# Optimization experiments

Hardware: AMD Instinct MI355X
Metric: run time of the kernel (lower is better)

Reference implementation:

```python
import jax, jax.numpy as jnp
import numpy as np

B, T, D, E, K = 4, 1024, 512, 10, 2
H = 4 * D          # expert hidden
CITY, CE = 8, 32   # num cities, city embedding dim
LIN = D + CE + D // 4 + D // 4 + D // 8 + D // 8  # 928 router input dim


def setup_inputs() -> dict:
    key = jax.random.key(0)
    ks = jax.random.split(key, 16)
    s = 0.02  # init scale for weights
    return {
        "x": jax.random.normal(ks[0], (B, T, D), jnp.float32),
        "delta_t": jax.random.normal(ks[1], (B, T, D // 4), jnp.float32),
        "delta_dis": jax.random.normal(ks[2], (B, T, D // 4), jnp.float32),
        "delta_rg": jax.random.normal(ks[3], (B, T, D // 8), jnp.float32),
        "delta_entropy": jax.random.normal(ks[4], (B, T, D // 8), jnp.float32),
        "city_emb": jax.random.normal(ks[5], (CITY, CE), jnp.float32),
        "Wg": jax.random.normal(ks[6], (E, LIN), jnp.float32) * s,
        "bg": jnp.zeros((E,), jnp.float32),
        "Wn": jax.random.normal(ks[7], (E, LIN), jnp.float32) * s,
        "bn": jnp.zeros((E,), jnp.float32),
        "W1": jax.random.normal(ks[8], (E, D, H), jnp.float32) * s,
        "b1": jnp.zeros((E, H), jnp.float32),
        "W2": jax.random.normal(ks[9], (E, H, D), jnp.float32) * s,
        "b2": jnp.zeros((E, D), jnp.float32),
        "noise": jax.random.normal(ks[10], (B, T, E), jnp.float32),
        "city": jax.random.randint(ks[11], (B,), 0, CITY),
    }


def reference(x, delta_t, delta_dis, delta_rg, delta_entropy, city_emb,
              Wg, bg, Wn, bn, W1, b1, W2, b2, noise, city):
    # ---- router: concat features -> noisy top-k gating ----
    ce = city_emb[city]                                   # (B, CE)
    ce = jnp.broadcast_to(ce[:, None, :], (x.shape[0], x.shape[1], ce.shape[-1]))
    h = jnp.concatenate([x, ce, delta_t, delta_dis, delta_rg, delta_entropy], axis=-1)  # (B,T,LIN)
    logits = jnp.einsum('btl,el->bte', h, Wg) + bg        # clean gate logits
    gate1 = jax.nn.softmax(logits, axis=-1)               # dense gate (returned for aux loss)
    noise_logits = jnp.einsum('btl,el->bte', h, Wn) + bn
    noisy = logits + noise * jax.nn.softplus(noise_logits)
    _, idx = jax.lax.top_k(noisy, K)                      # (B,T,K)
    sel = jax.nn.one_hot(idx, E, dtype=noisy.dtype).sum(-2) > 0  # (B,T,E) bool
    gating = jax.nn.softmax(jnp.where(sel, noisy, -jnp.inf), axis=-1)  # zeros off top-k

    # ---- experts: dense compute, combine weighted by sparse gate ----
    flat_x = x.reshape(-1, D)                             # (N, D)
    flat_g = gating.reshape(-1, E)                        # (N, E), zero for non-selected
    hid = jax.nn.gelu(jnp.einsum('nd,edh->neh', flat_x, W1) + b1, approximate=False)
    y = jnp.einsum('neh,ehd->ned', hid, W2) + b2          # (N, E, D)
    out = jnp.einsum('ne,ned->nd', flat_g, y).reshape(x.shape)
    return out, gate1
```

## Files before the change

### kernel.cpp

```cpp
#include <hip/hip_runtime.h>
#include <hip/hip_bf16.h>

#define B_      4
#define T_      1024
#define NTOK    4096
#define D_      512
#define E_      10
#define H_      2048
#define LIN_    928
#define TOPK    2
#define BM      128
#define ROWS_CAP 9472
#define TILES_CAP 74

typedef __bf16 bf16x8 __attribute__((ext_vector_type(8)));
typedef float  f32x4  __attribute__((ext_vector_type(4)));
typedef unsigned short ushort8 __attribute__((ext_vector_type(8)));

#define OFF_W1T   0ull
#define SZ_W1T    (10ull*2048*512*2)
#define OFF_W2T   (OFF_W1T + SZ_W1T)
#define SZ_W2T    SZ_W1T
#define OFF_XG    (OFF_W2T + SZ_W2T)
#define SZ_XG     ((size_t)ROWS_CAP*512*2)
#define OFF_HID   (OFF_XG + SZ_XG)
#define SZ_HID    ((size_t)ROWS_CAP*2048*2)
#define OFF_Y     OFF_W1T
#define OFF_TOKE  (OFF_HID + SZ_HID)
#define OFF_TOKG  (OFF_TOKE + 32768)
#define OFF_TROWS (OFF_TOKG + 32768)
#define OFF_RANK  (OFF_TROWS + 32768)
#define OFF_CNT   (OFF_RANK + 32768)
#define OFF_OFFS  (OFF_CNT + 64)
#define OFF_TE    (OFF_OFFS + 64)
#define OFF_TR    (OFF_TE + 512)

static __device__ __forceinline__ unsigned short f2b(float f) {
  unsigned int u = __float_as_uint(f);
  unsigned int r = (u + 0x7fffu + ((u >> 16) & 1u)) >> 16;
  return (unsigned short)r;
}

static __device__ __forceinline__ float b2f(unsigned short u) {
  return __uint_as_float(((unsigned int)u) << 16);
}

static __device__ __forceinline__ void gld16(const void* g, void* l) {
  __builtin_amdgcn_global_load_lds(
      (const __attribute__((address_space(1))) unsigned int*)g,
      (__attribute__((address_space(3))) unsigned int*)l, 16, 0, 0);
}

struct WconvLds { float t[64][65]; };

static __device__ __forceinline__ void wconv_body(
    const float* __restrict__ src, unsigned short* __restrict__ dst,
    int R, int C, int e, int bx, int by, int tid, WconvLds* W) {
  int c0 = bx << 6, r0 = by << 6;
  int rr = tid >> 4, cc = (tid & 15) << 2;
  const float* s = src + ((size_t)e * R + r0 + rr) * C + c0 + cc;
#pragma unroll
  for (int p = 0; p < 4; p++) {
    float4 v = *(const float4*)(s + (size_t)p * 16 * C);
    W->t[rr + p * 16][cc + 0] = v.x; W->t[rr + p * 16][cc + 1] = v.y;
    W->t[rr + p * 16][cc + 2] = v.z; W->t[rr + p * 16][cc + 3] = v.w;
  }
  __syncthreads();
  int wc2 = tid >> 2;
  unsigned short* d = dst + ((size_t)e * C + c0 + wc2) * R + r0;
#pragma unroll
  for (int p = 0; p < 4; p++) {
    int rb = ((tid & 3) << 2) + (p << 4);
    ushort4 o;
    o.x = f2b(W->t[rb + 0][wc2]); o.y = f2b(W->t[rb + 1][wc2]);
    o.z = f2b(W->t[rb + 2][wc2]); o.w = f2b(W->t[rb + 3][wc2]);
    *(ushort4*)&d[rb] = o;
  }
}

__global__ __launch_bounds__(256) void prep_k(
    const float* __restrict__ x, const float* __restrict__ dt,
    const float* __restrict__ dd, const float* __restrict__ dr,
    const float* __restrict__ de, const float* __restrict__ cemb,
    const int* __restrict__ city,
    const float* __restrict__ Wg, const float* __restrict__ Wn,
    const float* __restrict__ bg, const float* __restrict__ bn,
    const float* __restrict__ noise,
    const float* __restrict__ W1, const float* __restrict__ W2,
    unsigned short* __restrict__ w1T, unsigned short* __restrict__ w2T,
    float* __restrict__ gate1, int* __restrict__ tok_e,
    float* __restrict__ tok_g, int* __restrict__ ranks,
    int* __restrict__ counts) {
  __shared__ WconvLds W;
  __shared__ int lcnt[E_], lbase[E_];
  int bx = blockIdx.x;
  int tid = threadIdx.x;
  if (bx >= 256) {
    int idx = bx - 256;
    if (idx < 2560) wconv_body(W1, w1T, 512, 2048, idx / 256, idx & 31, (idx >> 5) & 7, tid, &W);
    else { idx -= 2560; wconv_body(W2, w2T, 2048, 512, idx / 256, idx & 7, (idx >> 3) & 31, tid, &W); }
    return;
  }
  if (tid < E_) lcnt[tid] = 0;
  __syncthreads();
  int lane = tid & 63;
  int gw = bx * 4 + (tid >> 6);
  int n0 = gw * 4;
  int cb = city[n0 >> 10];

  float acc[4][20];
#pragma unroll
  for (int j = 0; j < 4; j++)
#pragma unroll
    for (int o = 0; o < 20; o++) acc[j][o] = 0.f;

  {
    float hce = (lane < 32) ? cemb[cb * 32 + lane] : 0.f;
    int c = 512 + (lane & 31);
#pragma unroll
    for (int o = 0; o < 10; o++) {
      float wg = Wg[o * LIN_ + c];
      float wn = Wn[o * LIN_ + c];
#pragma unroll
      for (int j = 0; j < 4; j++) {
        acc[j][o]      = fmaf(hce, wg, acc[j][o]);
        acc[j][10 + o] = fmaf(hce, wn, acc[j][10 + o]);
      }
    }
  }
#pragma unroll
  for (int s = 0; s < 5; s++) {
    const float* hp; int Wd, cofs;
    if      (s == 0) { hp = x;  Wd = 512; cofs = 0;   }
    else if (s == 1) { hp = dt; Wd = 128; cofs = 544; }
    else if (s == 2) { hp = dd; Wd = 128; cofs = 672; }
    else if (s == 3) { hp = dr; Wd = 64;  cofs = 800; }
    else             { hp = de; Wd = 64;  cofs = 864; }
    for (int base = 0; base < Wd; base += 64) {
      int c = cofs + base + lane;
      float wv[20];
#pragma unroll
      for (int o = 0; o < 10; o++) {
        wv[o]      = Wg[o * LIN_ + c];
        wv[10 + o] = Wn[o * LIN_ + c];
      }
      float hv[4];
#pragma unroll
      for (int j = 0; j < 4; j++) hv[j] = hp[(size_t)(n0 + j) * Wd + base + lane];
#pragma unroll
      for (int j = 0; j < 4; j++)
#pragma unroll
        for (int o = 0; o < 20; o++) acc[j][o] = fmaf(hv[j], wv[o], acc[j][o]);
    }
  }
#pragma unroll
  for (int off = 1; off < 64; off <<= 1) {
#pragma unroll
    for (int j = 0; j < 4; j++)
#pragma unroll
      for (int o = 0; o < 20; o++) acc[j][o] += __shfl_xor(acc[j][o], off);
  }
  float sv[20];
#pragma unroll
  for (int o = 0; o < 20; o++) {
    float v = acc[0][o];
    v = (lane == 1) ? acc[1][o] : v;
    v = (lane == 2) ? acc[2][o] : v;
    v = (lane == 3) ? acc[3][o] : v;
    sv[o] = v;
  }
  int n = n0 + lane;
  int i0 = 0, i1 = 0, rr0 = 0, rr1 = 0;
  float gg0 = 0.f, gg1 = 0.f, gate[E_];
#pragma unroll
  for (int o = 0; o < E_; o++) gate[o] = 0.f;
  if (lane < 4) {
    float logits[E_], noisy[E_];
    float mx = -3.4e38f;
#pragma unroll
    for (int o = 0; o < E_; o++) { logits[o] = sv[o] + bg[o]; mx = fmaxf(mx, logits[o]); }
    float ssum = 0.f;
#pragma unroll
    for (int o = 0; o < E_; o++) { gate[o] = expf(logits[o] - mx); ssum += gate[o]; }
    float inv = 1.f / ssum;
#pragma unroll
    for (int o = 0; o < E_; o++) gate[o] *= inv;
#pragma unroll
    for (int o = 0; o < E_; o++) {
      float tt = sv[10 + o] + bn[o];
      float sp = (tt > 20.f) ? tt : log1pf(expf(tt));
      noisy[o] = logits[o] + noise[(size_t)n * E_ + o] * sp;
    }
    float v0 = noisy[0];
#pragma unroll
    for (int o = 1; o < E_; o++) if (noisy[o] > v0) { v0 = noisy[o]; i0 = o; }
    float v1 = -3.4e38f; i1 = -1;
#pragma unroll
    for (int o = 0; o < E_; o++) if (o != i0 && noisy[o] > v1) { v1 = noisy[o]; i1 = o; }
    float ee = expf(v1 - v0);
    gg0 = 1.f / (1.f + ee); gg1 = ee * gg0;
    rr0 = atomicAdd(&lcnt[i0], 1);
    rr1 = atomicAdd(&lcnt[i1], 1);
  }
  __syncthreads();
  if (tid < E_) lbase[tid] = atomicAdd(&counts[tid], lcnt[tid]);
  __syncthreads();
  if (lane < 4) {
    tok_e[2 * n] = i0;  tok_e[2 * n + 1] = i1;
    tok_g[2 * n] = gg0; tok_g[2 * n + 1] = gg1;
    ranks[2 * n]     = lbase[i0] + rr0;
    ranks[2 * n + 1] = lbase[i1] + rr1;
#pragma unroll
    for (int o = 0; o < E_; o++) gate1[(size_t)n * E_ + o] = gate[o];
  }
}

__global__ void setup_k(const int* __restrict__ counts, int* __restrict__ offsets,
                        int* __restrict__ tile_e, int* __restrict__ tile_r0) {
  __shared__ int cnt[E_], pf[E_ + 1], tb[E_ + 1];
  int tid = threadIdx.x;
  if (tid < E_) cnt[tid] = counts[tid];
  __syncthreads();
  if (tid == 0) {
    int off = 0, tt = 0;
    for (int e = 0; e < E_; e++) {
      pf[e] = off; tb[e] = tt;
      int nt = (cnt[e] + BM - 1) / BM;
      tt += nt; off += nt * BM;
    }
    pf[E_] = off; tb[E_] = tt;
  }
  __syncthreads();
  if (tid < E_) offsets[tid] = pf[tid];
  if (tid == E_) offsets[E_] = pf[E_];
  if (tid < TILES_CAP) {
    int e = -1;
#pragma unroll
    for (int k = 0; k < E_; k++) if (tid >= tb[k] && tid < tb[k + 1]) e = k;
    if (e >= 0) { tile_e[tid] = e; tile_r0[tid] = pf[e] + (tid - tb[e]) * BM; }
    else        { tile_e[tid] = -1; tile_r0[tid] = 0; }
  }
}

__global__ __launch_bounds__(256) void scatgath_k(
    const float* __restrict__ x, const int* __restrict__ tok_e,
    const int* __restrict__ ranks, const int* __restrict__ offsets,
    int* __restrict__ token_rows, unsigned short* __restrict__ xg) {
  int n = blockIdx.x * 4 + (threadIdx.x >> 6);
  int lane = threadIdx.x & 63;
  int e0 = tok_e[2 * n], e1 = tok_e[2 * n + 1];
  int p0 = offsets[e0] + ranks[2 * n];
  int p1 = offsets[e1] + ranks[2 * n + 1];
  if (lane == 0) { token_rows[2 * n] = p0; token_rows[2 * n + 1] = p1; }
  float4 a = *(const float4*)&x[(size_t)n * D_ + lane * 8];
  float4 b = *(const float4*)&x[(size_t)n * D_ + lane * 8 + 4];
  ushort8 o;
  o[0] = f2b(a.x); o[1] = f2b(a.y); o[2] = f2b(a.z); o[3] = f2b(a.w);
  o[4] = f2b(b.x); o[5] = f2b(b.y); o[6] = f2b(b.z); o[7] = f2b(b.w);
  *(ushort8*)&xg[(size_t)p0 * D_ + lane * 8] = o;
  *(ushort8*)&xg[(size_t)p1 * D_ + lane * 8] = o;
}

template<int KD, int ND, int GX, int MODE>
__global__ __launch_bounds__(256) void gemm_k(
    const unsigned short* __restrict__ A, const unsigned short* __restrict__ BT,
    const float* __restrict__ bias, unsigned short* __restrict__ outb,
    const int* __restrict__ tile_e, const int* __restrict__ tile_r0) {
  constexpr int BMT = 128, BNT = 128;
  constexpr int NT = KD / 32;
  constexpr int BUFSZ = (BMT + BNT) * 32;
  int nwg = GX * TILES_CAP;
  int fid = blockIdx.y * GX + blockIdx.x;
  int w = (fid & 7) * (nwg >> 3) + (fid >> 3);
  int bxs = w % GX, bys = w / GX;
  int e = tile_e[bys];
  if (e < 0) return;
  int row0 = tile_r0[bys];
  int n0 = bxs * BNT;
  int tid = threadIdx.x;
  int lane = tid & 63, wid = tid >> 6;
  int wr = wid >> 1, wc = wid & 1;
  __shared__ __align__(16) unsigned short LDS[3][BUFSZ];
  f32x4 acc[4][4] = {};
  const unsigned short* Ab = A + (size_t)row0 * KD;
  const unsigned short* Bb = BT + ((size_t)e * ND + n0) * KD;
  int lrow = lane >> 2, lcol = (lane & 3) * 8;
  int r = lane & 15, g8 = (lane >> 4) * 8;
  const unsigned short* gp[4];
  int loff[4];
#pragma unroll
  for (int i = 0; i < 4; i++) {
    int rowb = (wid + 4 * i) * 16;
    gp[i] = (rowb < BMT) ? Ab + (size_t)(rowb + lrow) * KD + lcol
                         : Bb + (size_t)(rowb - BMT + lrow) * KD + lcol;
    loff[i] = rowb * 32;
  }
  auto stage = [&](int buf) {
    unsigned short* lb = &LDS[0][0] + buf * BUFSZ;
#pragma unroll
    for (int i = 0; i < 4; i++) { gld16(gp[i], lb + loff[i]); gp[i] += 32; }
  };
  stage(0); stage(1);
  int cur = 0, nb = 2;
  for (int t = 0; t < NT; ++t) {
    if (t + 2 < NT) {
      stage(nb);
      asm volatile("s_waitcnt vmcnt(8)" ::: "memory");
    } else if (t + 2 == NT) {
      asm volatile("s_waitcnt vmcnt(4)" ::: "memory");
    } else {
      asm volatile("s_waitcnt vmcnt(0)" ::: "memory");
    }
    asm volatile("s_barrier" ::: "memory");
    const unsigned short* cb2 = &LDS[0][0] + cur * BUFSZ;
    bf16x8 av[4], bv[4];
#pragma unroll
    for (int mi = 0; mi < 4; mi++)
      av[mi] = *(const bf16x8*)&cb2[(wr * 64 + mi * 16 + r) * 32 + g8];
#pragma unroll
    for (int ni = 0; ni < 4; ni++)
      bv[ni] = *(const bf16x8*)&cb2[(BMT + wc * 64 + ni * 16 + r) * 32 + g8];
#pragma unroll
    for (int mi = 0; mi < 4; mi++)
#pragma unroll
      for (int ni = 0; ni < 4; ni++)
        acc[mi][ni] = __builtin_amdgcn_mfma_f32_16x16x32_bf16(av[mi], bv[ni], acc[mi][ni], 0, 0, 0);
    asm volatile("s_barrier" ::: "memory");
    cur = (cur == 2) ? 0 : cur + 1;
    nb = (nb == 2) ? 0 : nb + 1;
  }
  int rq = (lane >> 4) * 4;
#pragma unroll
  for (int mi = 0; mi < 4; mi++) {
#pragma unroll
    for (int ni = 0; ni < 4; ni++) {
      int col = n0 + wc * 64 + ni * 16 + r;
      float bz = (MODE == 0) ? bias[e * ND + col] : 0.f;
#pragma unroll
      for (int q = 0; q < 4; q++) {
        int row = row0 + wr * 64 + mi * 16 + rq + q;
        float v = acc[mi][ni][q];
        if constexpr (MODE == 0) {
          v += bz;
          v = 0.5f * v * (1.f + erff(v * 0.70710678118654752440f));
        }
        outb[(size_t)row * ND + col] = f2b(v);
      }
    }
  }
}

__global__ void combine_k(const unsigned short* __restrict__ y, const float* __restrict__ b2,
                          const int* __restrict__ token_rows, const int* __restrict__ tok_e,
                          const float* __restrict__ tok_g, float* __restrict__ out) {
  int gid = blockIdx.x * 256 + threadIdx.x;
  int n = gid >> 6;
  int c = (gid & 63) << 3;
  int r0 = token_rows[2 * n], r1 = token_rows[2 * n + 1];
  int e0 = tok_e[2 * n], e1 = tok_e[2 * n + 1];
  float g0 = tok_g[2 * n], g1 = tok_g[2 * n + 1];
  ushort8 y0 = *(const ushort8*)&y[(size_t)r0 * D_ + c];
  ushort8 y1 = *(const ushort8*)&y[(size_t)r1 * D_ + c];
  float ba[8], bb[8], o[8];
  *(float4*)&ba[0] = *(const float4*)&b2[e0 * D_ + c];
  *(float4*)&ba[4] = *(const float4*)&b2[e0 * D_ + c + 4];
  *(float4*)&bb[0] = *(const float4*)&b2[e1 * D_ + c];
  *(float4*)&bb[4] = *(const float4*)&b2[e1 * D_ + c + 4];
#pragma unroll
  for (int j = 0; j < 8; j++)
    o[j] = g0 * (b2f(y0[j]) + ba[j]) + g1 * (b2f(y1[j]) + bb[j]);
  *(float4*)&out[(size_t)n * D_ + c]     = *(float4*)&o[0];
  *(float4*)&out[(size_t)n * D_ + c + 4] = *(float4*)&o[4];
}

extern "C" void kernel_launch(void* const* d_in, const int* in_sizes, int n_in,
                              void* d_out, int out_size, void* d_ws, size_t ws_size,
                              hipStream_t stream) {
  const float* x     = (const float*)d_in[0];
  const float* dt    = (const float*)d_in[1];
  const float* dd    = (const float*)d_in[2];
  const float* dr    = (const float*)d_in[3];
  const float* de    = (const float*)d_in[4];
  const float* cemb  = (const float*)d_in[5];
  const float* Wg    = (const float*)d_in[6];
  const float* bg    = (const float*)d_in[7];
  const float* Wn    = (const float*)d_in[8];
  const float* bn    = (const float*)d_in[9];
  const float* W1    = (const float*)d_in[10];
  const float* b1    = (const float*)d_in[11];
  const float* W2    = (const float*)d_in[12];
  const float* b2    = (const float*)d_in[13];
  const float* noise = (const float*)d_in[14];
  const int*   city  = (const int*)d_in[15];

  float* out   = (float*)d_out;
  float* gate1 = out + (size_t)NTOK * D_;

  char* ws = (char*)d_ws;
  unsigned short* w1T  = (unsigned short*)(ws + OFF_W1T);
  unsigned short* w2T  = (unsigned short*)(ws + OFF_W2T);
  unsigned short* xg   = (unsigned short*)(ws + OFF_XG);
  unsigned short* hid  = (unsigned short*)(ws + OFF_HID);
  unsigned short* yb16 = (unsigned short*)(ws + OFF_Y);
  int*    tok_e       = (int*)(ws + OFF_TOKE);
  float*  tok_g       = (float*)(ws + OFF_TOKG);
  int*    token_rows  = (int*)(ws + OFF_TROWS);
  int*    ranks       = (int*)(ws + OFF_RANK);
  int*    counts      = (int*)(ws + OFF_CNT);
  int*    offsets     = (int*)(ws + OFF_OFFS);
  int*    tile_e      = (int*)(ws + OFF_TE);
  int*    tile_r0     = (int*)(ws + OFF_TR);

  hipMemsetAsync(counts, 0, E_ * sizeof(int), stream);
  prep_k<<<5376, 256, 0, stream>>>(x, dt, dd, dr, de, cemb, city, Wg, Wn, bg, bn,
                                   noise, W1, W2, w1T, w2T, gate1, tok_e, tok_g,
                                   ranks, counts);
  setup_k<<<1, 256, 0, stream>>>(counts, offsets, tile_e, tile_r0);
  scatgath_k<<<1024, 256, 0, stream>>>(x, tok_e, ranks, offsets, token_rows, xg);
  gemm_k<512, 2048, 16, 0><<<dim3(16, TILES_CAP), 256, 0, stream>>>(xg, w1T, b1, hid, tile_e, tile_r0);
  gemm_k<2048, 512, 4, 1><<<dim3(4, TILES_CAP), 256, 0, stream>>>(hid, w2T, nullptr, yb16, tile_e, tile_r0);
  combine_k<<<1024, 256, 0, stream>>>(yb16, b2, token_rows, tok_e, tok_g, out);
}
```

Before: 135.2 us.

## Remove setup kernel by recomputing expert offsets inline; widen bf16 transpose stores

Drops the single-block setup kernel. Each scatter/gather and GEMM block now recomputes expert row offsets and its tile-to-expert mapping from the ten counts, which removes one dependent launch from the serial chain. The weight-transpose epilogue also changes to write 8 bf16 values per store instead of 4. In exchange, every block does a small redundant prefix loop over the counts.

```diff
diff --git a/kernel.cpp b/kernel.cpp
--- a/kernel.cpp
+++ b/kernel.cpp
@@ -31,9 +31,6 @@
 #define OFF_TROWS (OFF_TOKG + 32768)
 #define OFF_RANK  (OFF_TROWS + 32768)
 #define OFF_CNT   (OFF_RANK + 32768)
-#define OFF_OFFS  (OFF_CNT + 64)
-#define OFF_TE    (OFF_OFFS + 64)
-#define OFF_TR    (OFF_TE + 512)
 
 static __device__ __forceinline__ unsigned short f2b(float f) {
   unsigned int u = __float_as_uint(f);
@@ -66,15 +63,14 @@
     W->t[rr + p * 16][cc + 2] = v.z; W->t[rr + p * 16][cc + 3] = v.w;
   }
   __syncthreads();
-  int wc2 = tid >> 2;
-  unsigned short* d = dst + ((size_t)e * C + c0 + wc2) * R + r0;
-#pragma unroll
-  for (int p = 0; p < 4; p++) {
-    int rb = ((tid & 3) << 2) + (p << 4);
-    ushort4 o;
-    o.x = f2b(W->t[rb + 0][wc2]); o.y = f2b(W->t[rb + 1][wc2]);
-    o.z = f2b(W->t[rb + 2][wc2]); o.w = f2b(W->t[rb + 3][wc2]);
-    *(ushort4*)&d[rb] = o;
+  int rb = (tid & 7) * 8;
+#pragma unroll
+  for (int pass = 0; pass < 2; pass++) {
+    int wc2 = pass * 32 + (tid >> 3);
+    ushort8 o;
+#pragma unroll
+    for (int i = 0; i < 8; i++) o[i] = f2b(W->t[rb + i][wc2]);
+    *(ushort8*)&dst[((size_t)e * C + c0 + wc2) * R + r0 + rb] = o;
   }
 }
 
@@ -215,42 +211,22 @@
   }
 }
 
-__global__ void setup_k(const int* __restrict__ counts, int* __restrict__ offsets,
-                        int* __restrict__ tile_e, int* __restrict__ tile_r0) {
-  __shared__ int cnt[E_], pf[E_ + 1], tb[E_ + 1];
-  int tid = threadIdx.x;
-  if (tid < E_) cnt[tid] = counts[tid];
-  __syncthreads();
-  if (tid == 0) {
-    int off = 0, tt = 0;
-    for (int e = 0; e < E_; e++) {
-      pf[e] = off; tb[e] = tt;
-      int nt = (cnt[e] + BM - 1) / BM;
-      tt += nt; off += nt * BM;
-    }
-    pf[E_] = off; tb[E_] = tt;
-  }
-  __syncthreads();
-  if (tid < E_) offsets[tid] = pf[tid];
-  if (tid == E_) offsets[E_] = pf[E_];
-  if (tid < TILES_CAP) {
-    int e = -1;
-#pragma unroll
-    for (int k = 0; k < E_; k++) if (tid >= tb[k] && tid < tb[k + 1]) e = k;
-    if (e >= 0) { tile_e[tid] = e; tile_r0[tid] = pf[e] + (tid - tb[e]) * BM; }
-    else        { tile_e[tid] = -1; tile_r0[tid] = 0; }
-  }
-}
-
 __global__ __launch_bounds__(256) void scatgath_k(
     const float* __restrict__ x, const int* __restrict__ tok_e,
-    const int* __restrict__ ranks, const int* __restrict__ offsets,
+    const int* __restrict__ ranks, const int* __restrict__ counts,
     int* __restrict__ token_rows, unsigned short* __restrict__ xg) {
   int n = blockIdx.x * 4 + (threadIdx.x >> 6);
   int lane = threadIdx.x & 63;
   int e0 = tok_e[2 * n], e1 = tok_e[2 * n + 1];
-  int p0 = offsets[e0] + ranks[2 * n];
-  int p1 = offsets[e1] + ranks[2 * n + 1];
+  int off0 = 0, off1 = 0, off = 0;
+#pragma unroll
+  for (int k = 0; k < E_; k++) {
+    if (k == e0) off0 = off;
+    if (k == e1) off1 = off;
+    off += ((counts[k] + BM - 1) / BM) * BM;
+  }
+  int p0 = off0 + ranks[2 * n];
+  int p1 = off1 + ranks[2 * n + 1];
   if (lane == 0) { token_rows[2 * n] = p0; token_rows[2 * n + 1] = p1; }
   float4 a = *(const float4*)&x[(size_t)n * D_ + lane * 8];
   float4 b = *(const float4*)&x[(size_t)n * D_ + lane * 8 + 4];
@@ -265,7 +241,7 @@
 __global__ __launch_bounds__(256) void gemm_k(
     const unsigned short* __restrict__ A, const unsigned short* __restrict__ BT,
     const float* __restrict__ bias, unsigned short* __restrict__ outb,
-    const int* __restrict__ tile_e, const int* __restrict__ tile_r0) {
+    const int* __restrict__ counts) {
   constexpr int BMT = 128, BNT = 128;
   constexpr int NT = KD / 32;
   constexpr int BUFSZ = (BMT + BNT) * 32;
@@ -273,9 +249,17 @@
   int fid = blockIdx.y * GX + blockIdx.x;
   int w = (fid & 7) * (nwg >> 3) + (fid >> 3);
   int bxs = w % GX, bys = w / GX;
-  int e = tile_e[bys];
+  int e = -1, row0 = 0;
+  {
+    int off = 0, tt = 0;
+#pragma unroll
+    for (int k = 0; k < E_; k++) {
+      int nt = (counts[k] + BM - 1) / BM;
+      if (bys >= tt && bys < tt + nt) { e = k; row0 = off + (bys - tt) * BM; }
+      tt += nt; off += nt * BM;
+    }
+  }
   if (e < 0) return;
-  int row0 = tile_r0[bys];
   int n0 = bxs * BNT;
   int tid = threadIdx.x;
   int lane = tid & 63, wid = tid >> 6;
@@ -407,17 +391,13 @@
   int*    token_rows  = (int*)(ws + OFF_TROWS);
   int*    ranks       = (int*)(ws + OFF_RANK);
   int*    counts      = (int*)(ws + OFF_CNT);
-  int*    offsets     = (int*)(ws + OFF_OFFS);
-  int*    tile_e      = (int*)(ws + OFF_TE);
-  int*    tile_r0     = (int*)(ws + OFF_TR);
 
   hipMemsetAsync(counts, 0, E_ * sizeof(int), stream);
   prep_k<<<5376, 256, 0, stream>>>(x, dt, dd, dr, de, cemb, city, Wg, Wn, bg, bn,
                                    noise, W1, W2, w1T, w2T, gate1, tok_e, tok_g,
                                    ranks, counts);
-  setup_k<<<1, 256, 0, stream>>>(counts, offsets, tile_e, tile_r0);
-  scatgath_k<<<1024, 256, 0, stream>>>(x, tok_e, ranks, offsets, token_rows, xg);
-  gemm_k<512, 2048, 16, 0><<<dim3(16, TILES_CAP), 256, 0, stream>>>(xg, w1T, b1, hid, tile_e, tile_r0);
-  gemm_k<2048, 512, 4, 1><<<dim3(4, TILES_CAP), 256, 0, stream>>>(hid, w2T, nullptr, yb16, tile_e, tile_r0);
+  scatgath_k<<<1024, 256, 0, stream>>>(x, tok_e, ranks, counts, token_rows, xg);
+  gemm_k<512, 2048, 16, 0><<<dim3(16, TILES_CAP), 256, 0, stream>>>(xg, w1T, b1, hid, counts);
+  gemm_k<2048, 512, 4, 1><<<dim3(4, TILES_CAP), 256, 0, stream>>>(hid, w2T, nullptr, yb16, counts);
   combine_k<<<1024, 256, 0, stream>>>(yb16, b2, token_rows, tok_e, tok_g, out);
 }
```

Result: no change. 135.4 us (+0.2%).
